# Kernel optimization log

Measured on AMD Instinct MI355X. Metric: run time of the kernel, lower is better.

Reference implementation:

```python
import jax, jax.numpy as jnp
import numpy as np

CLAMP_MIN = 1e-12
CLAMP_MAX = 1e12


def setup_inputs() -> dict:
    key = jax.random.key(0)
    k1, k2, k3 = jax.random.split(key, 3)
    N, C, H, W = 32, 11, 384, 384
    x = jax.random.normal(k1, (N, C, H, W), dtype=jnp.float32)
    centers = jax.random.normal(k2, (N, C, H, W), dtype=jnp.float32)
    labels = jax.random.randint(k3, (N, H, W), 0, C, dtype=jnp.int64)
    return {"x": x, "centers": centers, "labels": labels}


def reference(x, centers, labels):
    # x, centers: (N, C, H, W); labels: (N, H, W) int
    N, C, H, W = x.shape
    # res[n,c] = x[n,c]^2 + centers[n,c]^2 - 2 * x[n,c] @ centers[n,c]
    # (single batched matmul replaces the original per-(i,j) addmm loop)
    res = x * x + centers * centers - 2.0 * jnp.matmul(x, centers)
    # softmax over class dim, then max over class dim -> (N, H, W)
    res_max = jnp.max(jax.nn.softmax(res, axis=1), axis=1)
    dist = res_max * labels.astype(res_max.dtype)
    loss = jnp.sum(jnp.clip(dist, CLAMP_MIN, CLAMP_MAX)) / (H * W * N)
    return loss
```

## Files before the change

### kernel.cpp

```cpp
#include <hip/hip_runtime.h>
#include <stdint.h>

typedef __attribute__((ext_vector_type(8))) short short8;
typedef __attribute__((ext_vector_type(4))) float floatx4;
typedef __attribute__((ext_vector_type(4))) unsigned short u16x4;

#define Hh 384
#define Ww 384
#define Cc 11
#define Nn 32
#define PITCH 72

__device__ __forceinline__ unsigned short f2bf(float f) {
  union { float f; uint32_t u; } z; z.f = f;
  return (unsigned short)(z.u >> 16);
}
__device__ __forceinline__ float bf2f(unsigned short b) {
  union { uint32_t u; float f; } z; z.u = ((uint32_t)b) << 16;
  return z.f;
}

#define BAR() do {                                          \
    asm volatile("s_waitcnt lgkmcnt(0)" ::: "memory");      \
    __builtin_amdgcn_s_barrier();                           \
    asm volatile("" ::: "memory");                          \
  } while (0)

__global__ __launch_bounds__(256, 4)
void center_loss(const float* __restrict__ X, const float* __restrict__ Cen,
                 const int* __restrict__ Lab, float* __restrict__ Out) {
  __shared__ __align__(16) unsigned short Alds[2][64 * PITCH];
  __shared__ __align__(16) unsigned short Blds[2][64 * PITCH];
  __shared__ float red[4];

  const int bx   = blockIdx.x;
  const int xcd  = bx & 7;
  const int slot = bx >> 3;
  const int grp  = slot / 36;
  const int t36  = slot - grp * 36;
  const int n    = xcd + (grp << 3);
  const int ib = t36 / 6;
  const int jb = t36 - ib * 6;
  const int i0 = ib << 6, j0 = jb << 6;

  const int t   = threadIdx.x;
  const int l   = t & 63;
  const int w   = t >> 6;
  const int wr  = (w >> 1) << 5;
  const int wc  = (w & 1) << 5;
  const int q4  = l >> 4;
  const int l16 = l & 15;
  const int sr  = t >> 4;
  const int sa  = t & 15;
  const int jp  = t & 31;
  const int kc  = t >> 5;

  const size_t plane = (size_t)Hh * Ww;
  const float* xrow = X   + (size_t)n * Cc * plane + (size_t)(i0 + sr) * Ww + (sa << 2);
  const float* crow = Cen + (size_t)n * Cc * plane + (size_t)(kc << 3) * Ww + j0 + (jp << 1);

  float m[16], s[16];
#pragma unroll
  for (int i = 0; i < 16; ++i) { m[i] = -3.0e38f; s[i] = 0.0f; }

  floatx4 acc[2][2];
#pragma unroll
  for (int a = 0; a < 2; ++a)
#pragma unroll
    for (int b = 0; b < 2; ++b) acc[a][b] = (floatx4){0.f, 0.f, 0.f, 0.f};

  float4 pa[4];
  float2 pb[8];

#define LOADT(CC, KK) do {                                                     \
    const float* ap_ = xrow + (size_t)(CC) * plane + ((KK) << 6);              \
    pa[0] = *reinterpret_cast<const float4*>(ap_);                             \
    pa[1] = *reinterpret_cast<const float4*>(ap_ + 16 * Ww);                   \
    pa[2] = *reinterpret_cast<const float4*>(ap_ + 32 * Ww);                   \
    pa[3] = *reinterpret_cast<const float4*>(ap_ + 48 * Ww);                   \
    const float* bp_ = crow + (size_t)(CC) * plane + (size_t)((KK) << 6) * Ww; \
    _Pragma("unroll")                                                          \
    for (int u_ = 0; u_ < 8; ++u_)                                             \
      pb[u_] = *reinterpret_cast<const float2*>(bp_ + (size_t)u_ * Ww);        \
  } while (0)

#define STAGE(WB) do {                                                         \
    _Pragma("unroll")                                                          \
    for (int p_ = 0; p_ < 4; ++p_) {                                           \
      u16x4 pk_;                                                               \
      pk_.x = f2bf(pa[p_].x); pk_.y = f2bf(pa[p_].y);                          \
      pk_.z = f2bf(pa[p_].z); pk_.w = f2bf(pa[p_].w);                          \
      *reinterpret_cast<u16x4*>(&Alds[WB][(sr + 16 * p_) * PITCH + (sa << 2)]) = pk_; \
    }                                                                          \
    short8 s0_, s1_;                                                           \
    _Pragma("unroll")                                                          \
    for (int u_ = 0; u_ < 8; ++u_) {                                           \
      s0_[u_] = (short)f2bf(pb[u_].x);                                         \
      s1_[u_] = (short)f2bf(pb[u_].y);                                         \
    }                                                                          \
    *reinterpret_cast<short8*>(&Blds[WB][(jp << 1) * PITCH + (kc << 3)]) = s0_;       \
    *reinterpret_cast<short8*>(&Blds[WB][((jp << 1) + 1) * PITCH + (kc << 3)]) = s1_; \
  } while (0)

#define COMPUTE(RB) do {                                                       \
    if (kb == jb) {                       \
      _Pragma("unroll") for (int fr_ = 0; fr_ < 2; ++fr_)                      \
      _Pragma("unroll") for (int fc_ = 0; fc_ < 2; ++fc_)                      \
      _Pragma("unroll") for (int r_ = 0; r_ < 4; ++r_) {                       \
        const int pr_ = wr + (fr_ << 4) + (q4 << 2) + r_;                      \
        const int pc_ = wc + (fc_ << 4) + l16;                                 \
        float xv_ = bf2f(Alds[RB][pr_ * PITCH + pc_]);                         \
        acc[fr_][fc_][r_] -= 0.5f * xv_ * xv_;                                 \
      }                                                                        \
    }                                                                          \
    if (kb == ib) {         \
      _Pragma("unroll") for (int fr_ = 0; fr_ < 2; ++fr_)                      \
      _Pragma("unroll") for (int fc_ = 0; fc_ < 2; ++fc_)                      \
      _Pragma("unroll") for (int r_ = 0; r_ < 4; ++r_) {                       \
        const int pr_ = wr + (fr_ << 4) + (q4 << 2) + r_;                      \
        const int pc_ = wc + (fc_ << 4) + l16;                                 \
        float cv_ = bf2f(Blds[RB][pc_ * PITCH + pr_]);                         \
        acc[fr_][fc_][r_] -= 0.5f * cv_ * cv_;                                 \
      }                                                                        \
    }                                                                          \
    _Pragma("unroll") for (int ks_ = 0; ks_ < 2; ++ks_) {                      \
      const int ko_ = (ks_ << 5) + (q4 << 3);                                  \
      short8 a0_ = *reinterpret_cast<const short8*>(&Alds[RB][(wr +      l16) * PITCH + ko_]); \
      short8 a1_ = *reinterpret_cast<const short8*>(&Alds[RB][(wr + 16 + l16) * PITCH + ko_]); \
      short8 b0_ = *reinterpret_cast<const short8*>(&Blds[RB][(wc +      l16) * PITCH + ko_]); \
      short8 b1_ = *reinterpret_cast<const short8*>(&Blds[RB][(wc + 16 + l16) * PITCH + ko_]); \
      acc[0][0] = __builtin_amdgcn_mfma_f32_16x16x32_bf16(a0_, b0_, acc[0][0], 0, 0, 0); \
      acc[0][1] = __builtin_amdgcn_mfma_f32_16x16x32_bf16(a0_, b1_, acc[0][1], 0, 0, 0); \
      acc[1][0] = __builtin_amdgcn_mfma_f32_16x16x32_bf16(a1_, b0_, acc[1][0], 0, 0, 0); \
      acc[1][1] = __builtin_amdgcn_mfma_f32_16x16x32_bf16(a1_, b1_, acc[1][1], 0, 0, 0); \
    }                                                                          \
    if (kb == 5) {                \
      _Pragma("unroll") for (int fr_ = 0; fr_ < 2; ++fr_)                      \
      _Pragma("unroll") for (int fc_ = 0; fc_ < 2; ++fc_)                      \
      _Pragma("unroll") for (int r_ = 0; r_ < 4; ++r_) {                       \
        const int idx_ = ((fr_ << 1) + fc_) * 4 + r_;                          \
        float res_ = -2.0f * acc[fr_][fc_][r_];                                \
        float mi_ = m[idx_];                                                   \
        if (res_ <= mi_) {                                                     \
          s[idx_] += __expf(res_ - mi_);                                       \
        } else {                                                               \
          s[idx_] = s[idx_] * __expf(mi_ - res_) + 1.0f;                       \
          m[idx_] = res_;                                                      \
        }                                                                      \
        acc[fr_][fc_][r_] = 0.0f;                                              \
      }                                                                        \
    }                                                                          \
    ++kb; if (kb == 6) kb = 0;                                                 \
  } while (0)

  LOADT(0, 0);
  STAGE(0);
  LOADT(0, 1);
  BAR();

  int kb = 0;
  int kbL = 2, cL = 0;

  for (int mi = 0; mi < 32; ++mi) {
    STAGE(1);
    LOADT(cL, kbL);
    ++kbL; if (kbL == 6) { kbL = 0; ++cL; }
    COMPUTE(0);
    BAR();
    STAGE(0);
    LOADT(cL, kbL);
    ++kbL; if (kbL == 6) { kbL = 0; ++cL; }
    COMPUTE(1);
    BAR();
  }
  STAGE(1);
  COMPUTE(0);
  BAR();
  COMPUTE(1);

  float local = 0.0f;
  const int* lb = Lab + (size_t)n * plane;
#pragma unroll
  for (int fr = 0; fr < 2; ++fr)
#pragma unroll
    for (int fc = 0; fc < 2; ++fc)
#pragma unroll
      for (int r = 0; r < 4; ++r) {
        const int idx = ((fr << 1) + fc) * 4 + r;
        const int pr = i0 + wr + (fr << 4) + (q4 << 2) + r;
        const int pc = j0 + wc + (fc << 4) + l16;
        float val = 1.0f / s[idx];
        float d = val * (float)lb[pr * Ww + pc];
        d = fminf(fmaxf(d, 1e-12f), 1e12f);
        local += d;
      }
#pragma unroll
  for (int off = 32; off > 0; off >>= 1) local += __shfl_down(local, off, 64);
  if (l == 0) red[w] = local;
  __syncthreads();
  if (t == 0) {
    float bs = (red[0] + red[1] + red[2] + red[3]) * (1.0f / 4718592.0f);
    atomicAdd(Out, bs);
  }
}

extern "C" void kernel_launch(void* const* d_in, const int* in_sizes, int n_in,
                              void* d_out, int out_size, void* d_ws, size_t ws_size,
                              hipStream_t stream) {
  const float* X   = (const float*)d_in[0];
  const float* Cen = (const float*)d_in[1];
  const int*   Lab = (const int*)d_in[2];
  float* Out = (float*)d_out;
  hipMemsetAsync(Out, 0, (size_t)out_size * sizeof(float), stream);
  hipLaunchKernelGGL(center_loss, dim3(Nn * 36), dim3(256), 0, stream,
                     X, Cen, Lab, Out);
}
```

Baseline: 506.6 us.

## Use 512-thread blocks with single-buffered XOR-swizzled LDS tiles

Doubles the block to 8 waves, each computing a 32x16 slice of the 64x64 output tile, and drops LDS double buffering in favour of a single buffer with two barriers per k-step. LDS rows are XOR-swizzled so the 16-byte fragment reads and the transposed B writes avoid bank conflicts, and each thread now loads contiguous 8-float A segments and single B columns. The aim is higher occupancy and latency hiding with fewer conflicts. The cost is an extra barrier per iteration, since the load-to-compute overlap of the old double buffer is lost.

```diff
diff --git a/kernel.cpp b/kernel.cpp
--- a/kernel.cpp
+++ b/kernel.cpp
@@ -3,7 +3,6 @@
 
 typedef __attribute__((ext_vector_type(8))) short short8;
 typedef __attribute__((ext_vector_type(4))) float floatx4;
-typedef __attribute__((ext_vector_type(4))) unsigned short u16x4;
 
 #define Hh 384
 #define Ww 384
@@ -26,12 +25,12 @@
     asm volatile("" ::: "memory");                          \
   } while (0)
 
-__global__ __launch_bounds__(256, 4)
+__global__ __launch_bounds__(512, 8)
 void center_loss(const float* __restrict__ X, const float* __restrict__ Cen,
                  const int* __restrict__ Lab, float* __restrict__ Out) {
-  __shared__ __align__(16) unsigned short Alds[2][64 * PITCH];
-  __shared__ __align__(16) unsigned short Blds[2][64 * PITCH];
-  __shared__ float red[4];
+  __shared__ __align__(16) unsigned short Alds[64 * PITCH];
+  __shared__ __align__(16) unsigned short Blds[64 * PITCH];
+  __shared__ float red[8];
 
   const int bx   = blockIdx.x;
   const int xcd  = bx & 7;
@@ -46,100 +45,91 @@
   const int t   = threadIdx.x;
   const int l   = t & 63;
   const int w   = t >> 6;
-  const int wr  = (w >> 1) << 5;
-  const int wc  = (w & 1) << 5;
+  const int wr  = (w >> 2) << 5;
+  const int wc  = (w & 3) << 4;
   const int q4  = l >> 4;
   const int l16 = l & 15;
-  const int sr  = t >> 4;
-  const int sa  = t & 15;
-  const int jp  = t & 31;
-  const int kc  = t >> 5;
+  const int e8  = l16 & 7;
+  const int ar  = t >> 3;
+  const int ac  = t & 7;
+  const int aoff = ar * PITCH + ((ac ^ (ar & 7)) << 3);
+  const int boff = l * PITCH + ((w ^ (l & 7)) << 3);
+
+  const int fa0[2] = { (wr +      l16) * PITCH + (((0 + q4) ^ e8) << 3),
+                       (wr +      l16) * PITCH + (((4 + q4) ^ e8) << 3) };
+  const int fa1[2] = { (wr + 16 + l16) * PITCH + (((0 + q4) ^ e8) << 3),
+                       (wr + 16 + l16) * PITCH + (((4 + q4) ^ e8) << 3) };
+  const int fb0[2] = { (wc +      l16) * PITCH + (((0 + q4) ^ e8) << 3),
+                       (wc +      l16) * PITCH + (((4 + q4) ^ e8) << 3) };
 
   const size_t plane = (size_t)Hh * Ww;
-  const float* xrow = X   + (size_t)n * Cc * plane + (size_t)(i0 + sr) * Ww + (sa << 2);
-  const float* crow = Cen + (size_t)n * Cc * plane + (size_t)(kc << 3) * Ww + j0 + (jp << 1);
+  const float* xrow = X   + (size_t)n * Cc * plane + (size_t)(i0 + ar) * Ww + (ac << 3);
+  const float* crow = Cen + (size_t)n * Cc * plane + (size_t)(w << 3) * Ww + j0 + l;
 
-  float m[16], s[16];
+  float m[8], s[8];
 #pragma unroll
-  for (int i = 0; i < 16; ++i) { m[i] = -3.0e38f; s[i] = 0.0f; }
+  for (int i = 0; i < 8; ++i) { m[i] = -3.0e38f; s[i] = 0.0f; }
+  floatx4 acc[2];
+  acc[0] = (floatx4){0.f, 0.f, 0.f, 0.f};
+  acc[1] = (floatx4){0.f, 0.f, 0.f, 0.f};
 
-  floatx4 acc[2][2];
-#pragma unroll
-  for (int a = 0; a < 2; ++a)
-#pragma unroll
-    for (int b = 0; b < 2; ++b) acc[a][b] = (floatx4){0.f, 0.f, 0.f, 0.f};
-
-  float4 pa[4];
-  float2 pb[8];
+  float4 pa[2];
+  float  pb[8];
 
 #define LOADT(CC, KK) do {                                                     \
     const float* ap_ = xrow + (size_t)(CC) * plane + ((KK) << 6);              \
     pa[0] = *reinterpret_cast<const float4*>(ap_);                             \
-    pa[1] = *reinterpret_cast<const float4*>(ap_ + 16 * Ww);                   \
-    pa[2] = *reinterpret_cast<const float4*>(ap_ + 32 * Ww);                   \
-    pa[3] = *reinterpret_cast<const float4*>(ap_ + 48 * Ww);                   \
+    pa[1] = *reinterpret_cast<const float4*>(ap_ + 4);                         \
     const float* bp_ = crow + (size_t)(CC) * plane + (size_t)((KK) << 6) * Ww; \
     _Pragma("unroll")                                                          \
-    for (int u_ = 0; u_ < 8; ++u_)                                             \
-      pb[u_] = *reinterpret_cast<const float2*>(bp_ + (size_t)u_ * Ww);        \
+    for (int u_ = 0; u_ < 8; ++u_) pb[u_] = bp_[(size_t)u_ * Ww];              \
   } while (0)
 
-#define STAGE(WB) do {                                                         \
+#define STAGE() do {                                                           \
+    short8 av_;                                                                \
     _Pragma("unroll")                                                          \
-    for (int p_ = 0; p_ < 4; ++p_) {                                           \
-      u16x4 pk_;                                                               \
-      pk_.x = f2bf(pa[p_].x); pk_.y = f2bf(pa[p_].y);                          \
-      pk_.z = f2bf(pa[p_].z); pk_.w = f2bf(pa[p_].w);                          \
-      *reinterpret_cast<u16x4*>(&Alds[WB][(sr + 16 * p_) * PITCH + (sa << 2)]) = pk_; \
+    for (int i_ = 0; i_ < 4; ++i_) {                                           \
+      av_[i_]     = (short)f2bf(pa[0][i_]);                                    \
+      av_[i_ + 4] = (short)f2bf(pa[1][i_]);                                    \
     }                                                                          \
-    short8 s0_, s1_;                                                           \
+    *reinterpret_cast<short8*>(&Alds[aoff]) = av_;                             \
+    short8 bv_;                                                                \
     _Pragma("unroll")                                                          \
-    for (int u_ = 0; u_ < 8; ++u_) {                                           \
-      s0_[u_] = (short)f2bf(pb[u_].x);                                         \
-      s1_[u_] = (short)f2bf(pb[u_].y);                                         \
-    }                                                                          \
-    *reinterpret_cast<short8*>(&Blds[WB][(jp << 1) * PITCH + (kc << 3)]) = s0_;       \
-    *reinterpret_cast<short8*>(&Blds[WB][((jp << 1) + 1) * PITCH + (kc << 3)]) = s1_; \
+    for (int u_ = 0; u_ < 8; ++u_) bv_[u_] = (short)f2bf(pb[u_]);              \
+    *reinterpret_cast<short8*>(&Blds[boff]) = bv_;                             \
   } while (0)
 
-#define COMPUTE(RB) do {                                                       \
-    if (kb == jb) {                       \
+#define COMPUTE() do {                                                         \
+    if (kbC == jb) {            \
       _Pragma("unroll") for (int fr_ = 0; fr_ < 2; ++fr_)                      \
-      _Pragma("unroll") for (int fc_ = 0; fc_ < 2; ++fc_)                      \
       _Pragma("unroll") for (int r_ = 0; r_ < 4; ++r_) {                       \
         const int pr_ = wr + (fr_ << 4) + (q4 << 2) + r_;                      \
-        const int pc_ = wc + (fc_ << 4) + l16;                                 \
-        float xv_ = bf2f(Alds[RB][pr_ * PITCH + pc_]);                         \
-        acc[fr_][fc_][r_] -= 0.5f * xv_ * xv_;                                 \
+        const int pc_ = wc + l16;                                              \
+        float xv_ = bf2f(Alds[pr_ * PITCH + (((pc_ >> 3) ^ (pr_ & 7)) << 3) + (pc_ & 7)]); \
+        acc[fr_][r_] -= 0.5f * xv_ * xv_;                                      \
       }                                                                        \
     }                                                                          \
-    if (kb == ib) {         \
+    if (kbC == ib) {   \
       _Pragma("unroll") for (int fr_ = 0; fr_ < 2; ++fr_)                      \
-      _Pragma("unroll") for (int fc_ = 0; fc_ < 2; ++fc_)                      \
       _Pragma("unroll") for (int r_ = 0; r_ < 4; ++r_) {                       \
         const int pr_ = wr + (fr_ << 4) + (q4 << 2) + r_;                      \
-        const int pc_ = wc + (fc_ << 4) + l16;                                 \
-        float cv_ = bf2f(Blds[RB][pc_ * PITCH + pr_]);                         \
-        acc[fr_][fc_][r_] -= 0.5f * cv_ * cv_;                                 \
+        const int pc_ = wc + l16;                                              \
+        float cv_ = bf2f(Blds[pc_ * PITCH + (((pr_ >> 3) ^ (pc_ & 7)) << 3) + (pr_ & 7)]); \
+        acc[fr_][r_] -= 0.5f * cv_ * cv_;                                      \
       }                                                                        \
     }                                                                          \
     _Pragma("unroll") for (int ks_ = 0; ks_ < 2; ++ks_) {                      \
-      const int ko_ = (ks_ << 5) + (q4 << 3);                                  \
-      short8 a0_ = *reinterpret_cast<const short8*>(&Alds[RB][(wr +      l16) * PITCH + ko_]); \
-      short8 a1_ = *reinterpret_cast<const short8*>(&Alds[RB][(wr + 16 + l16) * PITCH + ko_]); \
-      short8 b0_ = *reinterpret_cast<const short8*>(&Blds[RB][(wc +      l16) * PITCH + ko_]); \
-      short8 b1_ = *reinterpret_cast<const short8*>(&Blds[RB][(wc + 16 + l16) * PITCH + ko_]); \
-      acc[0][0] = __builtin_amdgcn_mfma_f32_16x16x32_bf16(a0_, b0_, acc[0][0], 0, 0, 0); \
-      acc[0][1] = __builtin_amdgcn_mfma_f32_16x16x32_bf16(a0_, b1_, acc[0][1], 0, 0, 0); \
-      acc[1][0] = __builtin_amdgcn_mfma_f32_16x16x32_bf16(a1_, b0_, acc[1][0], 0, 0, 0); \
-      acc[1][1] = __builtin_amdgcn_mfma_f32_16x16x32_bf16(a1_, b1_, acc[1][1], 0, 0, 0); \
+      short8 a0_ = *reinterpret_cast<const short8*>(&Alds[fa0[ks_]]);          \
+      short8 a1_ = *reinterpret_cast<const short8*>(&Alds[fa1[ks_]]);          \
+      short8 b0_ = *reinterpret_cast<const short8*>(&Blds[fb0[ks_]]);          \
+      acc[0] = __builtin_amdgcn_mfma_f32_16x16x32_bf16(a0_, b0_, acc[0], 0, 0, 0); \
+      acc[1] = __builtin_amdgcn_mfma_f32_16x16x32_bf16(a1_, b0_, acc[1], 0, 0, 0); \
     }                                                                          \
-    if (kb == 5) {                \
+    if (kbC == 5) {               \
       _Pragma("unroll") for (int fr_ = 0; fr_ < 2; ++fr_)                      \
-      _Pragma("unroll") for (int fc_ = 0; fc_ < 2; ++fc_)                      \
       _Pragma("unroll") for (int r_ = 0; r_ < 4; ++r_) {                       \
-        const int idx_ = ((fr_ << 1) + fc_) * 4 + r_;                          \
-        float res_ = -2.0f * acc[fr_][fc_][r_];                                \
+        const int idx_ = (fr_ << 2) + r_;                                      \
+        float res_ = -2.0f * acc[fr_][r_];                                     \
         float mi_ = m[idx_];                                                   \
         if (res_ <= mi_) {                                                     \
           s[idx_] += __expf(res_ - mi_);                                       \
@@ -147,59 +137,49 @@
           s[idx_] = s[idx_] * __expf(mi_ - res_) + 1.0f;                       \
           m[idx_] = res_;                                                      \
         }                                                                      \
-        acc[fr_][fc_][r_] = 0.0f;                                              \
+        acc[fr_][r_] = 0.0f;                                                   \
       }                                                                        \
     }                                                                          \
-    ++kb; if (kb == 6) kb = 0;                                                 \
   } while (0)
 
   LOADT(0, 0);
-  STAGE(0);
-  LOADT(0, 1);
-  BAR();
 
-  int kb = 0;
-  int kbL = 2, cL = 0;
+  int kbC = 0;
+  int kbL = 1, cL = 0;
 
-  for (int mi = 0; mi < 32; ++mi) {
-    STAGE(1);
-    LOADT(cL, kbL);
-    ++kbL; if (kbL == 6) { kbL = 0; ++cL; }
-    COMPUTE(0);
+  for (int it = 0; it < 66; ++it) {
     BAR();
-    STAGE(0);
-    LOADT(cL, kbL);
-    ++kbL; if (kbL == 6) { kbL = 0; ++cL; }
-    COMPUTE(1);
+    STAGE();
+    if (it < 65) {
+      LOADT(cL, kbL);
+      ++kbL; if (kbL == 6) { kbL = 0; ++cL; }
+    }
     BAR();
+    COMPUTE();
+    ++kbC; if (kbC == 6) kbC = 0;
   }
-  STAGE(1);
-  COMPUTE(0);
-  BAR();
-  COMPUTE(1);
 
   float local = 0.0f;
   const int* lb = Lab + (size_t)n * plane;
 #pragma unroll
   for (int fr = 0; fr < 2; ++fr)
 #pragma unroll
-    for (int fc = 0; fc < 2; ++fc)
-#pragma unroll
-      for (int r = 0; r < 4; ++r) {
-        const int idx = ((fr << 1) + fc) * 4 + r;
-        const int pr = i0 + wr + (fr << 4) + (q4 << 2) + r;
-        const int pc = j0 + wc + (fc << 4) + l16;
-        float val = 1.0f / s[idx];
-        float d = val * (float)lb[pr * Ww + pc];
-        d = fminf(fmaxf(d, 1e-12f), 1e12f);
-        local += d;
-      }
+    for (int r = 0; r < 4; ++r) {
+      const int idx = (fr << 2) + r;
+      const int pr = i0 + wr + (fr << 4) + (q4 << 2) + r;
+      const int pc = j0 + wc + l16;
+      float val = 1.0f / s[idx];
+      float d = val * (float)lb[pr * Ww + pc];
+      d = fminf(fmaxf(d, 1e-12f), 1e12f);
+      local += d;
+    }
 #pragma unroll
   for (int off = 32; off > 0; off >>= 1) local += __shfl_down(local, off, 64);
   if (l == 0) red[w] = local;
   __syncthreads();
   if (t == 0) {
-    float bs = (red[0] + red[1] + red[2] + red[3]) * (1.0f / 4718592.0f);
+    float bs = (red[0] + red[1] + red[2] + red[3] +
+                red[4] + red[5] + red[6] + red[7]) * (1.0f / 4718592.0f);
     atomicAdd(Out, bs);
   }
 }
@@ -212,6 +192,6 @@
   const int*   Lab = (const int*)d_in[2];
   float* Out = (float*)d_out;
   hipMemsetAsync(Out, 0, (size_t)out_size * sizeof(float), stream);
-  hipLaunchKernelGGL(center_loss, dim3(Nn * 36), dim3(256), 0, stream,
+  hipLaunchKernelGGL(center_loss, dim3(Nn * 36), dim3(512), 0, stream,
                      X, Cen, Lab, Out);
 }
```

Result: slower. 656.0 us (+29.5%).

## Single-buffer LDS with register double-buffering and coalesced B loads

Applied to the files above, without the earlier changes.

Replaces the double-buffered LDS tiles with a single LDS buffer. The next tile is instead prefetched into a second set of registers, with extra barriers around staging and compute. The B (centers) loads become per-lane scalar loads coalesced along the row, with packed bf16 conversion done through a byte permute. The online softmax update becomes branchless, and launch bounds drop to 3 blocks per CU. The changes target load coalescing and divergence, but they add barriers per tile and carry more registers, which could reduce occupancy.

```diff
diff --git a/kernel.cpp b/kernel.cpp
--- a/kernel.cpp
+++ b/kernel.cpp
@@ -3,7 +3,8 @@
 
 typedef __attribute__((ext_vector_type(8))) short short8;
 typedef __attribute__((ext_vector_type(4))) float floatx4;
-typedef __attribute__((ext_vector_type(4))) unsigned short u16x4;
+typedef __attribute__((ext_vector_type(2))) uint32_t u32x2;
+typedef __attribute__((ext_vector_type(4))) uint32_t u32x4;
 
 #define Hh 384
 #define Ww 384
@@ -11,13 +12,13 @@
 #define Nn 32
 #define PITCH 72
 
-__device__ __forceinline__ unsigned short f2bf(float f) {
-  union { float f; uint32_t u; } z; z.f = f;
-  return (unsigned short)(z.u >> 16);
-}
 __device__ __forceinline__ float bf2f(unsigned short b) {
   union { uint32_t u; float f; } z; z.u = ((uint32_t)b) << 16;
   return z.f;
+}
+__device__ __forceinline__ uint32_t pkbf(float hi, float lo) {
+  union { float f; uint32_t u; } a, b; a.f = hi; b.f = lo;
+  return __builtin_amdgcn_perm(a.u, b.u, 0x07060302u);
 }
 
 #define BAR() do {                                          \
@@ -26,11 +27,11 @@
     asm volatile("" ::: "memory");                          \
   } while (0)
 
-__global__ __launch_bounds__(256, 4)
+__global__ __launch_bounds__(256, 3)
 void center_loss(const float* __restrict__ X, const float* __restrict__ Cen,
                  const int* __restrict__ Lab, float* __restrict__ Out) {
-  __shared__ __align__(16) unsigned short Alds[2][64 * PITCH];
-  __shared__ __align__(16) unsigned short Blds[2][64 * PITCH];
+  __shared__ __align__(16) unsigned short Alds[64 * PITCH];
+  __shared__ __align__(16) unsigned short Blds[64 * PITCH];
   __shared__ float red[4];
 
   const int bx   = blockIdx.x;
@@ -50,14 +51,15 @@
   const int wc  = (w & 1) << 5;
   const int q4  = l >> 4;
   const int l16 = l & 15;
+  const int sa  = t & 15;
   const int sr  = t >> 4;
-  const int sa  = t & 15;
-  const int jp  = t & 31;
-  const int kc  = t >> 5;
 
   const size_t plane = (size_t)Hh * Ww;
-  const float* xrow = X   + (size_t)n * Cc * plane + (size_t)(i0 + sr) * Ww + (sa << 2);
-  const float* crow = Cen + (size_t)n * Cc * plane + (size_t)(kc << 3) * Ww + j0 + (jp << 1);
+  const float* xbase = X   + (size_t)n * Cc * plane;
+  const float* cbase = Cen + (size_t)n * Cc * plane;
+  const size_t aoffg = (size_t)(i0 + sr) * Ww + (sa << 2);
+  const size_t boffg0 = (size_t)((w << 3) +  0) * Ww + j0 + l;
+  const size_t boffg1 = (size_t)((w << 3) + 32) * Ww + j0 + l;
 
   float m[16], s[16];
 #pragma unroll
@@ -69,114 +71,110 @@
 #pragma unroll
     for (int b = 0; b < 2; ++b) acc[a][b] = (floatx4){0.f, 0.f, 0.f, 0.f};
 
-  float4 pa[4];
-  float2 pb[8];
-
-#define LOADT(CC, KK) do {                                                     \
-    const float* ap_ = xrow + (size_t)(CC) * plane + ((KK) << 6);              \
-    pa[0] = *reinterpret_cast<const float4*>(ap_);                             \
-    pa[1] = *reinterpret_cast<const float4*>(ap_ + 16 * Ww);                   \
-    pa[2] = *reinterpret_cast<const float4*>(ap_ + 32 * Ww);                   \
-    pa[3] = *reinterpret_cast<const float4*>(ap_ + 48 * Ww);                   \
-    const float* bp_ = crow + (size_t)(CC) * plane + (size_t)((KK) << 6) * Ww; \
-    _Pragma("unroll")                                                          \
-    for (int u_ = 0; u_ < 8; ++u_)                                             \
-      pb[u_] = *reinterpret_cast<const float2*>(bp_ + (size_t)u_ * Ww);        \
-  } while (0)
-
-#define STAGE(WB) do {                                                         \
+  float4 pa[4], na[4];
+  float  pb[16], nb[16];
+
+#define LOADT(PA, PB, CC, KK) do {                                             \
+    const float* ap_ = xbase + (size_t)(CC) * plane + ((KK) << 6) + aoffg;     \
+    PA[0] = *reinterpret_cast<const float4*>(ap_);                             \
+    PA[1] = *reinterpret_cast<const float4*>(ap_ + (size_t)16 * Ww);           \
+    PA[2] = *reinterpret_cast<const float4*>(ap_ + (size_t)32 * Ww);           \
+    PA[3] = *reinterpret_cast<const float4*>(ap_ + (size_t)48 * Ww);           \
+    const float* b0_ = cbase + (size_t)(CC) * plane + (size_t)((KK) << 6) * Ww;\
+    const float* bp0 = b0_ + boffg0;                                           \
+    const float* bp1 = b0_ + boffg1;                                           \
+    _Pragma("unroll")                                                          \
+    for (int u_ = 0; u_ < 8; ++u_) PB[u_]     = bp0[(size_t)u_ * Ww];          \
+    _Pragma("unroll")                                                          \
+    for (int u_ = 0; u_ < 8; ++u_) PB[8 + u_] = bp1[(size_t)u_ * Ww];          \
+  } while (0)
+
+#define STAGE(PA, PB) do {                                                     \
     _Pragma("unroll")                                                          \
     for (int p_ = 0; p_ < 4; ++p_) {                                           \
-      u16x4 pk_;                                                               \
-      pk_.x = f2bf(pa[p_].x); pk_.y = f2bf(pa[p_].y);                          \
-      pk_.z = f2bf(pa[p_].z); pk_.w = f2bf(pa[p_].w);                          \
-      *reinterpret_cast<u16x4*>(&Alds[WB][(sr + 16 * p_) * PITCH + (sa << 2)]) = pk_; \
-    }                                                                          \
-    short8 s0_, s1_;                                                           \
-    _Pragma("unroll")                                                          \
-    for (int u_ = 0; u_ < 8; ++u_) {                                           \
-      s0_[u_] = (short)f2bf(pb[u_].x);                                         \
-      s1_[u_] = (short)f2bf(pb[u_].y);                                         \
-    }                                                                          \
-    *reinterpret_cast<short8*>(&Blds[WB][(jp << 1) * PITCH + (kc << 3)]) = s0_;       \
-    *reinterpret_cast<short8*>(&Blds[WB][((jp << 1) + 1) * PITCH + (kc << 3)]) = s1_; \
-  } while (0)
-
-#define COMPUTE(RB) do {                                                       \
-    if (kb == jb) {                       \
+      u32x2 pk_;                                                               \
+      pk_.x = pkbf(PA[p_].y, PA[p_].x);                                        \
+      pk_.y = pkbf(PA[p_].w, PA[p_].z);                                        \
+      *reinterpret_cast<u32x2*>(&Alds[(sr + 16 * p_) * PITCH + (sa << 2)]) = pk_; \
+    }                                                                          \
+    _Pragma("unroll")                                                          \
+    for (int p_ = 0; p_ < 2; ++p_) {                                           \
+      u32x4 pk_;                                                               \
+      pk_.x = pkbf(PB[p_ * 8 + 1], PB[p_ * 8 + 0]);                            \
+      pk_.y = pkbf(PB[p_ * 8 + 3], PB[p_ * 8 + 2]);                            \
+      pk_.z = pkbf(PB[p_ * 8 + 5], PB[p_ * 8 + 4]);                            \
+      pk_.w = pkbf(PB[p_ * 8 + 7], PB[p_ * 8 + 6]);                            \
+      *reinterpret_cast<u32x4*>(&Blds[l * PITCH + (w << 3) + (p_ << 5)]) = pk_;\
+    }                                                                          \
+  } while (0)
+
+#define COMPUTE() do {                                                         \
+    if (kb == jb) {                             \
       _Pragma("unroll") for (int fr_ = 0; fr_ < 2; ++fr_)                      \
       _Pragma("unroll") for (int fc_ = 0; fc_ < 2; ++fc_)                      \
       _Pragma("unroll") for (int r_ = 0; r_ < 4; ++r_) {                       \
         const int pr_ = wr + (fr_ << 4) + (q4 << 2) + r_;                      \
         const int pc_ = wc + (fc_ << 4) + l16;                                 \
-        float xv_ = bf2f(Alds[RB][pr_ * PITCH + pc_]);                         \
+        float xv_ = bf2f(Alds[pr_ * PITCH + pc_]);                             \
         acc[fr_][fc_][r_] -= 0.5f * xv_ * xv_;                                 \
       }                                                                        \
     }                                                                          \
-    if (kb == ib) {         \
+    if (kb == ib) {                          \
       _Pragma("unroll") for (int fr_ = 0; fr_ < 2; ++fr_)                      \
       _Pragma("unroll") for (int fc_ = 0; fc_ < 2; ++fc_)                      \
       _Pragma("unroll") for (int r_ = 0; r_ < 4; ++r_) {                       \
         const int pr_ = wr + (fr_ << 4) + (q4 << 2) + r_;                      \
         const int pc_ = wc + (fc_ << 4) + l16;                                 \
-        float cv_ = bf2f(Blds[RB][pc_ * PITCH + pr_]);                         \
+        float cv_ = bf2f(Blds[pc_ * PITCH + pr_]);                             \
         acc[fr_][fc_][r_] -= 0.5f * cv_ * cv_;                                 \
       }                                                                        \
     }                                                                          \
     _Pragma("unroll") for (int ks_ = 0; ks_ < 2; ++ks_) {                      \
       const int ko_ = (ks_ << 5) + (q4 << 3);                                  \
-      short8 a0_ = *reinterpret_cast<const short8*>(&Alds[RB][(wr +      l16) * PITCH + ko_]); \
-      short8 a1_ = *reinterpret_cast<const short8*>(&Alds[RB][(wr + 16 + l16) * PITCH + ko_]); \
-      short8 b0_ = *reinterpret_cast<const short8*>(&Blds[RB][(wc +      l16) * PITCH + ko_]); \
-      short8 b1_ = *reinterpret_cast<const short8*>(&Blds[RB][(wc + 16 + l16) * PITCH + ko_]); \
+      short8 a0_ = *reinterpret_cast<const short8*>(&Alds[(wr +      l16) * PITCH + ko_]); \
+      short8 a1_ = *reinterpret_cast<const short8*>(&Alds[(wr + 16 + l16) * PITCH + ko_]); \
+      short8 b0_ = *reinterpret_cast<const short8*>(&Blds[(wc +      l16) * PITCH + ko_]); \
+      short8 b1_ = *reinterpret_cast<const short8*>(&Blds[(wc + 16 + l16) * PITCH + ko_]); \
       acc[0][0] = __builtin_amdgcn_mfma_f32_16x16x32_bf16(a0_, b0_, acc[0][0], 0, 0, 0); \
       acc[0][1] = __builtin_amdgcn_mfma_f32_16x16x32_bf16(a0_, b1_, acc[0][1], 0, 0, 0); \
       acc[1][0] = __builtin_amdgcn_mfma_f32_16x16x32_bf16(a1_, b0_, acc[1][0], 0, 0, 0); \
       acc[1][1] = __builtin_amdgcn_mfma_f32_16x16x32_bf16(a1_, b1_, acc[1][1], 0, 0, 0); \
     }                                                                          \
-    if (kb == 5) {                \
+    if (kb == 5) {            \
       _Pragma("unroll") for (int fr_ = 0; fr_ < 2; ++fr_)                      \
       _Pragma("unroll") for (int fc_ = 0; fc_ < 2; ++fc_)                      \
       _Pragma("unroll") for (int r_ = 0; r_ < 4; ++r_) {                       \
         const int idx_ = ((fr_ << 1) + fc_) * 4 + r_;                          \
         float res_ = -2.0f * acc[fr_][fc_][r_];                                \
-        float mi_ = m[idx_];                                                   \
-        if (res_ <= mi_) {                                                     \
-          s[idx_] += __expf(res_ - mi_);                                       \
-        } else {                                                               \
-          s[idx_] = s[idx_] * __expf(mi_ - res_) + 1.0f;                       \
-          m[idx_] = res_;                                                      \
-        }                                                                      \
+        float M_ = fmaxf(m[idx_], res_);                                       \
+        s[idx_] = s[idx_] * __expf(m[idx_] - M_) + __expf(res_ - M_);          \
+        m[idx_] = M_;                                                          \
         acc[fr_][fc_][r_] = 0.0f;                                              \
       }                                                                        \
     }                                                                          \
-    ++kb; if (kb == 6) kb = 0;                                                 \
-  } while (0)
-
-  LOADT(0, 0);
-  STAGE(0);
-  LOADT(0, 1);
-  BAR();
-
-  int kb = 0;
-  int kbL = 2, cL = 0;
-
-  for (int mi = 0; mi < 32; ++mi) {
-    STAGE(1);
-    LOADT(cL, kbL);
+    ++kb; if (kb == 6) { kb = 0; ++c; }                                        \
+  } while (0)
+
+  LOADT(pa, pb, 0, 0);
+  int kb = 0, c = 0;
+  int kbL = 1, cL = 0;
+
+  for (int mi = 0; mi < 33; ++mi) {
+    BAR();
+    LOADT(na, nb, cL, kbL);
     ++kbL; if (kbL == 6) { kbL = 0; ++cL; }
-    COMPUTE(0);
-    BAR();
-    STAGE(0);
-    LOADT(cL, kbL);
-    ++kbL; if (kbL == 6) { kbL = 0; ++cL; }
-    COMPUTE(1);
-    BAR();
+    STAGE(pa, pb);
+    BAR();
+    COMPUTE();
+    BAR();
+    if (mi < 32) {
+      LOADT(pa, pb, cL, kbL);
+      ++kbL; if (kbL == 6) { kbL = 0; ++cL; }
+    }
+    STAGE(na, nb);
+    BAR();
+    COMPUTE();
   }
-  STAGE(1);
-  COMPUTE(0);
-  BAR();
-  COMPUTE(1);
 
   float local = 0.0f;
   const int* lb = Lab + (size_t)n * plane;
```

New measurement: 488.6 us. -3.6%, faster.
